# Kernel optimization log

Measured on AMD Instinct MI355X. Metric: run time of the kernel, lower is better.

## Reference

```python
import jax, jax.numpy as jnp
import numpy as np

NUM_SPLIT = 4

def setup_inputs() -> dict:
    key = jax.random.key(0)
    x = jax.random.normal(key, (8, 64, 256, 256), dtype=jnp.float32)
    return {"x": x}

def reference(x) -> jnp.ndarray:
    # x: [B, S*cell^2, H, W] with H == W. Per split group, channel index p within
    # a group maps to intra-block (row, col) = (p // cell, p % cell); block (h, w)
    # of the output is the cell x cell patch from spatial position (h, w).
    B, C, H, W = x.shape
    S = NUM_SPLIT
    cpg = C // S                      # channels per group = cell^2
    cell = int(round(np.sqrt(cpg)))
    # [B, S, cell_r, cell_c, H, W] -> [B, S, H, cell_r, W, cell_c] -> [B, S, H*cell, W*cell]
    out = x.reshape(B, S, cell, cell, H, W)
    out = out.transpose(0, 1, 4, 2, 5, 3)
    return out.reshape(B, S, H * cell, W * cell)
```

## Files before the change

kernel.cpp:

```cpp
#include <hip/hip_runtime.h>


#define TOTAL_ELEMS (8 * 64 * 256 * 256)
#define TOTAL_F4    (TOTAL_ELEMS / 4)
#define CH_STRIDE   65536

__global__ __launch_bounds__(256) void DepthToSpace_8486855377460_kernel(
    const float* __restrict__ in, float* __restrict__ out) {
    int idx4 = blockIdx.x * blockDim.x + threadIdx.x;
    int base = idx4 << 2;

    int ww = base & 1023;
    int hh = (base >> 10) & 1023;
    int s  = (base >> 20) & 3;
    int b  = base >> 22;

    int w = ww >> 2;
    int r = hh & 3;
    int h = hh >> 2;
    int c = (s << 4) + (r << 2);

    int in_off = (((b << 6) + c) << 16) + (h << 8) + w;

    float4 v;
    v.x = in[in_off];
    v.y = in[in_off + 1 * CH_STRIDE];
    v.z = in[in_off + 2 * CH_STRIDE];
    v.w = in[in_off + 3 * CH_STRIDE];

    reinterpret_cast<float4*>(out)[idx4] = v;
}

extern "C" void kernel_launch(void* const* d_in, const int* in_sizes, int n_in,
                              void* d_out, int out_size, void* d_ws, size_t ws_size,
                              hipStream_t stream) {
    const float* x = (const float*)d_in[0];
    float* out = (float*)d_out;
    dim3 block(256);
    dim3 grid(TOTAL_F4 / 256);
    DepthToSpace_8486855377460_kernel<<<grid, block, 0, stream>>>(x, out);
}
```

Baseline: 220.2 us.

## Load float4 from input and transpose 4x4 via cross-lane shuffles

Each thread now loads one float4 (four consecutive spatial positions of a single channel) instead of four scalar loads strided by a channel. A 4x4 transpose across groups of four lanes, done with two rounds of xor shuffles, puts the data into the output layout before a float4 store. This aims to make global reads fully vectorized and to cut the number of load instructions, at the cost of shuffle and select ALU work.

```diff
diff --git a/kernel.cpp b/kernel.cpp
--- a/kernel.cpp
+++ b/kernel.cpp
@@ -3,39 +3,53 @@
 
 #define TOTAL_ELEMS (8 * 64 * 256 * 256)
 #define TOTAL_F4    (TOTAL_ELEMS / 4)
-#define CH_STRIDE   65536
 
 __global__ __launch_bounds__(256) void DepthToSpace_8486855377460_kernel(
-    const float* __restrict__ in, float* __restrict__ out) {
-    int idx4 = blockIdx.x * blockDim.x + threadIdx.x;
-    int base = idx4 << 2;
+    const float4* __restrict__ in4, float4* __restrict__ out4) {
+    int o = blockIdx.x * 256 + threadIdx.x;
 
-    int ww = base & 1023;
-    int hh = (base >> 10) & 1023;
-    int s  = (base >> 20) & 3;
-    int b  = base >> 22;
+    int l  = o & 3;
+    int q  = (o >> 2) & 63;
+    int hh = (o >> 8) & 1023;
+    int s  = (o >> 18) & 3;
+    int b  = o >> 20;
 
-    int w = ww >> 2;
     int r = hh & 3;
     int h = hh >> 2;
-    int c = (s << 4) + (r << 2);
+    int p = (s << 4) + (r << 2) + l;
 
-    int in_off = (((b << 6) + c) << 16) + (h << 8) + w;
+    float4 m = in4[(((b << 6) + p) << 14) + (h << 6) + q];
 
+    int odd = l & 1;
+    float s0 = odd ? m.x : m.y;
+    float s1 = odd ? m.z : m.w;
+    float r0 = __shfl_xor(s0, 1, 64);
+    float r1 = __shfl_xor(s1, 1, 64);
+    float4 n;
+    n.x = odd ? r0  : m.x;
+    n.y = odd ? m.y : r0;
+    n.z = odd ? r1  : m.z;
+    n.w = odd ? m.w : r1;
+
+    int hi = l & 2;
+    s0 = hi ? n.x : n.z;
+    s1 = hi ? n.y : n.w;
+    r0 = __shfl_xor(s0, 2, 64);
+    r1 = __shfl_xor(s1, 2, 64);
     float4 v;
-    v.x = in[in_off];
-    v.y = in[in_off + 1 * CH_STRIDE];
-    v.z = in[in_off + 2 * CH_STRIDE];
-    v.w = in[in_off + 3 * CH_STRIDE];
+    v.x = hi ? r0  : n.x;
+    v.y = hi ? r1  : n.y;
+    v.z = hi ? n.z : r0;
+    v.w = hi ? n.w : r1;
 
-    reinterpret_cast<float4*>(out)[idx4] = v;
+    out4[o] = v;
 }
 
 extern "C" void kernel_launch(void* const* d_in, const int* in_sizes, int n_in,
                               void* d_out, int out_size, void* d_ws, size_t ws_size,
                               hipStream_t stream) {
-    const float* x = (const float*)d_in[0];
-    float* out = (float*)d_out;
+    const float4* x = (const float4*)d_in[0];
+    float4* out = (float4*)d_out;
     dim3 block(256);
     dim3 grid(TOTAL_F4 / 256);
     DepthToSpace_8486855377460_kernel<<<grid, block, 0, stream>>>(x, out);
```

Result: no change. 223.7 us (+1.6%).
